# Performance work log

Hardware: AMD Instinct MI355X
Metric: run time of the kernel (lower is better)

The kernel has to match this reference:

```python
import jax, jax.numpy as jnp
import numpy as np

EPS = 1e-5

def _bn_relu(x, g, b, m, v):
    # inference batchnorm + relu, NCHW, fused affine
    scale = g * jax.lax.rsqrt(v + EPS)
    shift = b - m * scale
    return jnp.maximum(x * scale[None, :, None, None] + shift[None, :, None, None], 0.0)

def _conv1x1(x, w):
    # x: [B,C,H,W], w: [O,C]
    return jnp.einsum('bchw,oc->bohw', x, w)

def _xcorr_depthwise(search, kernel, padding=0):
    # search: [B,C,Hs,Ws], kernel: [B,C,Hk,Wk]; grouped conv, groups=B*C
    B, C, Hs, Ws = search.shape
    Hk, Wk = kernel.shape[2], kernel.shape[3]
    x = search.reshape(1, B * C, Hs, Ws)
    k = kernel.reshape(B * C, 1, Hk, Wk)
    out = jax.lax.conv_general_dilated(
        x, k, window_strides=(1, 1), padding=[(padding, padding), (padding, padding)],
        feature_group_count=B * C, dimension_numbers=('NCHW', 'OIHW', 'NCHW'))
    return out.reshape(B, C, out.shape[2], out.shape[3])

def setup_inputs():
    key = jax.random.key(0)
    ks = jax.random.split(key, 20)
    B, Cin, HID, COUT = 128, 256, 256, 20
    s = 1.0 / np.sqrt(Cin)
    inp = {
        'kernel': jax.random.normal(ks[0], (B, Cin, 7, 7), jnp.float32),
        'search': jax.random.normal(ks[1], (B, Cin, 31, 31), jnp.float32),
        # conv_kernel branch (1x1 conv weight stored as [O,C]) + BN stats
        'w_k': jax.random.normal(ks[2], (HID, Cin), jnp.float32) * s,
        'g_k': 1.0 + 0.1 * jax.random.normal(ks[3], (HID,), jnp.float32),
        'b_k': 0.1 * jax.random.normal(ks[4], (HID,), jnp.float32),
        'm_k': 0.1 * jax.random.normal(ks[5], (HID,), jnp.float32),
        'v_k': jax.random.uniform(ks[6], (HID,), jnp.float32, 0.5, 1.5),
        # conv_search branch
        'w_s': jax.random.normal(ks[7], (HID, Cin), jnp.float32) * s,
        'g_s': 1.0 + 0.1 * jax.random.normal(ks[8], (HID,), jnp.float32),
        'b_s': 0.1 * jax.random.normal(ks[9], (HID,), jnp.float32),
        'm_s': 0.1 * jax.random.normal(ks[10], (HID,), jnp.float32),
        'v_s': jax.random.uniform(ks[11], (HID,), jnp.float32, 0.5, 1.5),
        # head: conv1(1x1)+BN+ReLU, conv2(1x1, bias)
        'w_h1': jax.random.normal(ks[12], (HID, HID), jnp.float32) * (1.0 / np.sqrt(HID)),
        'g_h': 1.0 + 0.1 * jax.random.normal(ks[13], (HID,), jnp.float32),
        'b_h': 0.1 * jax.random.normal(ks[14], (HID,), jnp.float32),
        'm_h': 0.1 * jax.random.normal(ks[15], (HID,), jnp.float32),
        'v_h': jax.random.uniform(ks[16], (HID,), jnp.float32, 0.5, 1.5),
        'w_h2': jax.random.normal(ks[17], (COUT, HID), jnp.float32) * (1.0 / np.sqrt(HID)),
        'bias_h2': 0.1 * jax.random.normal(ks[18], (COUT,), jnp.float32),
    }
    return inp

def reference(kernel, search, w_k, g_k, b_k, m_k, v_k, w_s, g_s, b_s, m_s, v_s,
              w_h1, g_h, b_h, m_h, v_h, w_h2, bias_h2):
    k = _bn_relu(_conv1x1(kernel, w_k), g_k, b_k, m_k, v_k)   # [B,256,7,7]
    s = _bn_relu(_conv1x1(search, w_s), g_s, b_s, m_s, v_s)   # [B,256,31,31]
    feat = _xcorr_depthwise(s, k, padding=0)                  # [B,256,25,25]
    y = _bn_relu(_conv1x1(feat, w_h1), g_h, b_h, m_h, v_h)
    out = _conv1x1(y, w_h2) + bias_h2[None, :, None, None]    # [B,20,25,25]
    return out
```

## Files before the change

### kernel.cpp

```cpp
#include <hip/hip_runtime.h>
#include <hip/hip_fp16.h>

typedef _Float16 f16;
typedef __attribute__((ext_vector_type(8))) _Float16 f16x8;
typedef __attribute__((ext_vector_type(4))) _Float16 f16x4;
typedef __attribute__((ext_vector_type(2))) _Float16 f16x2;
typedef __attribute__((ext_vector_type(4))) float f32x4;

#define MFMA16(a, b, c) __builtin_amdgcn_mfma_f32_16x16x32_f16((a), (b), (c), 0, 0, 0)

#define OFF_WK   0u
#define OFF_WS   131072u
#define OFF_WH1  262144u
#define OFF_W2P  393216u
#define OFF_SH   409600u
#define OFF_S    412672u
#define OFF_KF   63392768u

__global__ __launch_bounds__(256) void prep_weights(
    const float* __restrict__ wk, const float* __restrict__ gk, const float* __restrict__ bk,
    const float* __restrict__ mk, const float* __restrict__ vk,
    const float* __restrict__ wsr, const float* __restrict__ gs, const float* __restrict__ bs,
    const float* __restrict__ ms, const float* __restrict__ vs,
    const float* __restrict__ wh1, const float* __restrict__ gh, const float* __restrict__ bh,
    const float* __restrict__ mh, const float* __restrict__ vh,
    const float* __restrict__ wh2,
    f16* __restrict__ wk16, f16* __restrict__ ws16, f16* __restrict__ wh116,
    f16* __restrict__ w2p, float* __restrict__ shifts) {
  int o = blockIdx.x;
  int t = threadIdx.x;
  float sck = gk[o] * rsqrtf(vk[o] + 1e-5f);
  float scs = gs[o] * rsqrtf(vs[o] + 1e-5f);
  float sch = gh[o] * rsqrtf(vh[o] + 1e-5f);
  int idx = o * 256 + t;
  wk16[idx]  = (f16)(wk[idx] * sck);
  ws16[idx]  = (f16)(wsr[idx] * scs);
  wh116[idx] = (f16)(wh1[idx] * sch);
  if (o < 32) w2p[idx] = (o < 20) ? (f16)wh2[idx] : (f16)0;
  if (t == 0) {
    shifts[o]       = bk[o] - mk[o] * sck;
    shifts[256 + o] = bs[o] - ms[o] * scs;
    shifts[512 + o] = bh[o] - mh[o] * sch;
  }
}

__device__ __forceinline__ int pi_row(int q, int r) {
  return (q ^ (r << 2)) + (r << 4);
}
__device__ __forceinline__ int row128(int n) {
  return (n & 64) + pi_row((n >> 2) & 15, n & 3);
}

__global__ __launch_bounds__(512) void conv_nchw128(
    const float* __restrict__ X, const f16* __restrict__ W,
    const float* __restrict__ shift, f16* __restrict__ out) {
  const int C = 256, P = 961;
  int b = blockIdx.x >> 3;
  int ti = blockIdx.x & 7;
  int n0 = ti * 128; if (n0 > P - 128) n0 = P - 128;
  int t = threadIdx.x;
  int w = t >> 6, lane = t & 63;
  int fm = lane & 15, kg = lane >> 4;
  int wo = (w & 3) * 64;
  int wpx = (w >> 2) * 64;

  __shared__ f16 Bs[2][128 * 40];

  int px = (t & 31) * 4;
  int cpr = (t >> 5) * 2;
  const float* xb = X + ((size_t)b * C) * P + n0 + px;

  int wrow[4];
#pragma unroll
  for (int e = 0; e < 4; ++e) wrow[e] = row128(px + e);
  int rrow[4];
#pragma unroll
  for (int nf = 0; nf < 4; ++nf) rrow[nf] = row128(wpx + nf * 16 + fm);

  const f16* wp = W + (size_t)(wo + fm) * C + kg * 8;

  f32x4 rb[3][2];
#pragma unroll
  for (int s = 0; s < 3; ++s) {
    int cl = s * 32 + cpr;
    rb[s][0] = *(const f32x4*)(xb + (size_t)cl * P);
    rb[s][1] = *(const f32x4*)(xb + (size_t)(cl + 1) * P);
  }

  f32x4 acc[4][4] = {};
#pragma unroll
  for (int ci = 0; ci < 8; ++ci) {
    f16x8 a[4];
#pragma unroll
    for (int of = 0; of < 4; ++of)
      a[of] = *(const f16x8*)(wp + (size_t)of * 16 * C + ci * 32);

    f16* buf = Bs[ci & 1];
#pragma unroll
    for (int e = 0; e < 4; ++e) {
      f16x2 v;
      v[0] = (f16)rb[ci % 3][0][e];
      v[1] = (f16)rb[ci % 3][1][e];
      *(f16x2*)&buf[wrow[e] * 40 + cpr] = v;
    }
    if (ci + 3 < 8) {
      int cl = (ci + 3) * 32 + cpr;
      rb[ci % 3][0] = *(const f32x4*)(xb + (size_t)cl * P);
      rb[ci % 3][1] = *(const f32x4*)(xb + (size_t)(cl + 1) * P);
    }
    asm volatile("s_waitcnt lgkmcnt(0)" ::: "memory");
    __builtin_amdgcn_s_barrier();

    f16x8 bfr[4];
#pragma unroll
    for (int nf = 0; nf < 4; ++nf)
      bfr[nf] = *(const f16x8*)&buf[rrow[nf] * 40 + kg * 8];
#pragma unroll
    for (int of = 0; of < 4; ++of)
#pragma unroll
      for (int nf = 0; nf < 4; ++nf)
        acc[of][nf] = MFMA16(a[of], bfr[nf], acc[of][nf]);
  }

#pragma unroll
  for (int of = 0; of < 4; ++of) {
    int orow = wo + of * 16 + kg * 4;
    f32x4 sh = *(const f32x4*)(shift + orow);
#pragma unroll
    for (int nf = 0; nf < 4; ++nf) {
      int n = n0 + wpx + nf * 16 + fm;
      f16x4 st;
#pragma unroll
      for (int r = 0; r < 4; ++r)
        st[r] = (f16)fmaxf(acc[of][nf][r] + sh[r], 0.0f);
      *(f16x4*)(out + ((size_t)b * P + n) * C + orow) = st;
    }
  }
}

template <int P>
__global__ __launch_bounds__(256) void conv_nchw(
    const float* __restrict__ X, const f16* __restrict__ W,
    const float* __restrict__ shift, f16* __restrict__ out) {
  const int C = 256;
  int n0 = blockIdx.x * 64;
  int t = threadIdx.x;
  int lane = t & 63, wave = t >> 6;
  int fm = lane & 15, kg = lane >> 4;

  __shared__ f16 Bs[2][64 * 40];

  int b0 = n0 / P, bp0 = n0 - b0 * P;
  bool safe = (bp0 + 64 <= P);

  int px = (t & 15) * 4;
  int cpr = (t >> 4) * 2;
  const float* xb = X + ((size_t)b0 * C) * P + bp0 + px;

  int ub[4], up[4];
  if (!safe) {
#pragma unroll
    for (int e = 0; e < 4; ++e) {
      int gn = n0 + px + e;
      ub[e] = gn / P;
      up[e] = gn - ub[e] * P;
    }
  }

  int wrow[4];
#pragma unroll
  for (int e = 0; e < 4; ++e) wrow[e] = pi_row(t & 15, e);
  int rrow[4];
#pragma unroll
  for (int nf = 0; nf < 4; ++nf) rrow[nf] = pi_row(nf * 4 + (fm >> 2), fm & 3);

  const f16* wp = W + (size_t)(wave * 64 + fm) * C + kg * 8;

  f32x4 rb[3][2];
#pragma unroll
  for (int s = 0; s < 3; ++s) {
    int cl = s * 32 + cpr;
    if (safe) {
      rb[s][0] = *(const f32x4*)(xb + (size_t)cl * P);
      rb[s][1] = *(const f32x4*)(xb + (size_t)(cl + 1) * P);
    } else {
#pragma unroll
      for (int e = 0; e < 4; ++e) {
        rb[s][0][e] = X[((size_t)ub[e] * C + cl) * P + up[e]];
        rb[s][1][e] = X[((size_t)ub[e] * C + cl + 1) * P + up[e]];
      }
    }
  }

  f32x4 acc[4][4] = {};
#pragma unroll
  for (int ci = 0; ci < 8; ++ci) {
    f16x8 a[4];
#pragma unroll
    for (int of = 0; of < 4; ++of)
      a[of] = *(const f16x8*)(wp + (size_t)of * 16 * C + ci * 32);

    f16* buf = Bs[ci & 1];
#pragma unroll
    for (int e = 0; e < 4; ++e) {
      f16x2 v;
      v[0] = (f16)rb[ci % 3][0][e];
      v[1] = (f16)rb[ci % 3][1][e];
      *(f16x2*)&buf[wrow[e] * 40 + cpr] = v;
    }
    if (ci + 3 < 8) {
      int cl = (ci + 3) * 32 + cpr;
      if (safe) {
        rb[ci % 3][0] = *(const f32x4*)(xb + (size_t)cl * P);
        rb[ci % 3][1] = *(const f32x4*)(xb + (size_t)(cl + 1) * P);
      } else {
#pragma unroll
        for (int e = 0; e < 4; ++e) {
          rb[ci % 3][0][e] = X[((size_t)ub[e] * C + cl) * P + up[e]];
          rb[ci % 3][1][e] = X[((size_t)ub[e] * C + cl + 1) * P + up[e]];
        }
      }
    }
    asm volatile("s_waitcnt lgkmcnt(0)" ::: "memory");
    __builtin_amdgcn_s_barrier();

    f16x8 b[4];
#pragma unroll
    for (int nf = 0; nf < 4; ++nf)
      b[nf] = *(const f16x8*)&buf[rrow[nf] * 40 + kg * 8];
#pragma unroll
    for (int of = 0; of < 4; ++of)
#pragma unroll
      for (int nf = 0; nf < 4; ++nf)
        acc[of][nf] = MFMA16(a[of], b[nf], acc[of][nf]);
  }

#pragma unroll
  for (int of = 0; of < 4; ++of) {
    int orow = wave * 64 + of * 16 + kg * 4;
    f32x4 sh = *(const f32x4*)(shift + orow);
#pragma unroll
    for (int nf = 0; nf < 4; ++nf) {
      int n = n0 + nf * 16 + fm;
      f16x4 st;
#pragma unroll
      for (int r = 0; r < 4; ++r)
        st[r] = (f16)fmaxf(acc[of][nf][r] + sh[r], 0.0f);
      *(f16x4*)(out + (size_t)n * C + orow) = st;
    }
  }
}

__global__ __launch_bounds__(256) void xcorr_head(
    const f16* __restrict__ S ,
    const f16* __restrict__ Kf ,
    const f16* __restrict__ W1, const float* __restrict__ shift,
    const f16* __restrict__ W2p, const float* __restrict__ bias,
    float* __restrict__ out ) {
  const int C = 256;
  int id = blockIdx.x;
  int x = id & 7;
  int r = id >> 3;
  int g = r % 7;
  int b = (r / 7) * 8 + x;

  int t = threadIdx.x;
  int w = t >> 6, lane = t & 63;
  int fm = lane & 15, kg = lane >> 4;
  int oi = g * 4 + w;

  __shared__ char F[100 * 512];

  if (oi < 25) {
    const f16* Sb = S + (size_t)b * 961 * 256 + lane * 4;
    const f16* Kb = Kf + (size_t)b * 49 * 256 + lane * 4;
    f16x4 acc[25] = {};
    for (int di = 0; di < 7; ++di) {
      const f16* sp = Sb + (size_t)(oi + di) * 31 * 256;
      f16x4 srow[31];
#pragma unroll
      for (int j = 0; j < 31; ++j) srow[j] = *(const f16x4*)(sp + (size_t)j * 256);
      const f16* kp = Kb + (size_t)di * 7 * 256;
      f16x4 krow[7];
#pragma unroll
      for (int j = 0; j < 7; ++j) krow[j] = *(const f16x4*)(kp + (size_t)j * 256);
#pragma unroll
      for (int dj = 0; dj < 7; ++dj) {
        f16x4 kv = krow[dj];
#pragma unroll
        for (int oj = 0; oj < 25; ++oj)
          acc[oj] += srow[oj + dj] * kv;
      }
    }
#pragma unroll
    for (int oj = 0; oj < 25; ++oj) {
      int n = w * 25 + oj;
      *(f16x4*)(F + ((n * 512 + lane * 8) ^ ((n & 7) << 4))) = acc[oj];
    }
  } else {
    f16x4 z = {};
#pragma unroll
    for (int oj = 0; oj < 25; ++oj) {
      int n = w * 25 + oj;
      *(f16x4*)(F + ((n * 512 + lane * 8) ^ ((n & 7) << 4))) = z;
    }
  }
  __syncthreads();

  const f16* wp = W1 + (size_t)(w * 64 + fm) * C + kg * 8;
  f32x4 acc1[4][7] = {};
  f16x8 a_cur[4], a_nxt[4];
#pragma unroll
  for (int of = 0; of < 4; ++of)
    a_cur[of] = *(const f16x8*)(wp + (size_t)of * 16 * C);
#pragma unroll
  for (int ci = 0; ci < 8; ++ci) {
    if (ci < 7) {
#pragma unroll
      for (int of = 0; of < 4; ++of)
        a_nxt[of] = *(const f16x8*)(wp + (size_t)of * 16 * C + (ci + 1) * 32);
    }
    f16x8 bf[7];
#pragma unroll
    for (int nf = 0; nf < 7; ++nf) {
      int n = nf * 16 + fm;
      int rn = n < 100 ? n : n - 100;
      bf[nf] = *(const f16x8*)(F + ((rn * 512 + (ci * 32 + kg * 8) * 2) ^ ((rn & 7) << 4)));
    }
    __builtin_amdgcn_s_setprio(1);
#pragma unroll
    for (int of = 0; of < 4; ++of)
#pragma unroll
      for (int nf = 0; nf < 7; ++nf)
        acc1[of][nf] = MFMA16(a_cur[of], bf[nf], acc1[of][nf]);
    __builtin_amdgcn_s_setprio(0);
#pragma unroll
    for (int of = 0; of < 4; ++of) a_cur[of] = a_nxt[of];
  }
  __syncthreads();

#pragma unroll
  for (int of = 0; of < 4; ++of) {
    int orow = w * 64 + of * 16 + kg * 4;
    f32x4 sh = *(const f32x4*)(shift + orow);
#pragma unroll
    for (int nf = 0; nf < 7; ++nf) {
      int n = nf * 16 + fm;
      if (n < 100) {
        f16x4 st;
#pragma unroll
        for (int q = 0; q < 4; ++q)
          st[q] = (f16)fmaxf(acc1[of][nf][q] + sh[q], 0.0f);
        *(f16x4*)(F + ((n * 512 + orow * 2) ^ ((n & 7) << 4))) = st;
      }
    }
  }
  __syncthreads();

  f32x4 acc2[2][2] = {};
  int nfa = w, nfb = w + 4;
  f16x8 w2_cur[2], w2_nxt[2];
  w2_cur[0] = *(const f16x8*)(W2p + (size_t)fm * C + kg * 8);
  w2_cur[1] = *(const f16x8*)(W2p + (size_t)(16 + fm) * C + kg * 8);
#pragma unroll
  for (int ci = 0; ci < 8; ++ci) {
    if (ci < 7) {
      w2_nxt[0] = *(const f16x8*)(W2p + (size_t)fm * C + (ci + 1) * 32 + kg * 8);
      w2_nxt[1] = *(const f16x8*)(W2p + (size_t)(16 + fm) * C + (ci + 1) * 32 + kg * 8);
    }
    int na = nfa * 16 + fm;
    f16x8 b0 = *(const f16x8*)(F + ((na * 512 + (ci * 32 + kg * 8) * 2) ^ ((na & 7) << 4)));
    __builtin_amdgcn_s_setprio(1);
    acc2[0][0] = MFMA16(w2_cur[0], b0, acc2[0][0]);
    acc2[1][0] = MFMA16(w2_cur[1], b0, acc2[1][0]);
    __builtin_amdgcn_s_setprio(0);
    if (nfb < 7) {
      int nb = nfb * 16 + fm;
      int rnb = nb < 100 ? nb : nb - 100;
      f16x8 b1 = *(const f16x8*)(F + ((rnb * 512 + (ci * 32 + kg * 8) * 2) ^ ((rnb & 7) << 4)));
      __builtin_amdgcn_s_setprio(1);
      acc2[0][1] = MFMA16(w2_cur[0], b1, acc2[0][1]);
      acc2[1][1] = MFMA16(w2_cur[1], b1, acc2[1][1]);
      __builtin_amdgcn_s_setprio(0);
    }
    w2_cur[0] = w2_nxt[0];
    w2_cur[1] = w2_nxt[1];
  }

#pragma unroll
  for (int q = 0; q < 2; ++q) {
    int nf = q ? nfb : nfa;
    if (nf >= 7) continue;
    int n = nf * 16 + fm;
    if (n < 100) {
      int oi2 = g * 4 + n / 25;
      int oj2 = n % 25;
      if (oi2 < 25) {
        float* op = out + (size_t)b * 12500 + oi2 * 25 + oj2;
#pragma unroll
        for (int of = 0; of < 2; ++of)
#pragma unroll
          for (int e = 0; e < 4; ++e) {
            int o = of * 16 + kg * 4 + e;
            if (o < 20) op[(size_t)o * 625] = acc2[of][q][e] + bias[o];
          }
      }
    }
  }
}

extern "C" void kernel_launch(void* const* d_in, const int* in_sizes, int n_in,
                              void* d_out, int out_size, void* d_ws, size_t ws_size,
                              hipStream_t stream) {
  const float* kernel_in = (const float*)d_in[0];
  const float* search    = (const float*)d_in[1];
  const float* w_k = (const float*)d_in[2];
  const float* g_k = (const float*)d_in[3];
  const float* b_k = (const float*)d_in[4];
  const float* m_k = (const float*)d_in[5];
  const float* v_k = (const float*)d_in[6];
  const float* w_s = (const float*)d_in[7];
  const float* g_s = (const float*)d_in[8];
  const float* b_s = (const float*)d_in[9];
  const float* m_s = (const float*)d_in[10];
  const float* v_s = (const float*)d_in[11];
  const float* w_h1 = (const float*)d_in[12];
  const float* g_h = (const float*)d_in[13];
  const float* b_h = (const float*)d_in[14];
  const float* m_h = (const float*)d_in[15];
  const float* v_h = (const float*)d_in[16];
  const float* w_h2 = (const float*)d_in[17];
  const float* bias_h2 = (const float*)d_in[18];
  float* out = (float*)d_out;

  char* ws = (char*)d_ws;
  f16* wk16  = (f16*)(ws + OFF_WK);
  f16* ws16  = (f16*)(ws + OFF_WS);
  f16* wh116 = (f16*)(ws + OFF_WH1);
  f16* w2p   = (f16*)(ws + OFF_W2P);
  float* shifts = (float*)(ws + OFF_SH);
  f16* sbuf = (f16*)(ws + OFF_S);
  f16* kbuf = (f16*)(ws + OFF_KF);

  prep_weights<<<256, 256, 0, stream>>>(w_k, g_k, b_k, m_k, v_k,
                                        w_s, g_s, b_s, m_s, v_s,
                                        w_h1, g_h, b_h, m_h, v_h, w_h2,
                                        wk16, ws16, wh116, w2p, shifts);

  conv_nchw128<<<dim3(1024), 512, 0, stream>>>(search, ws16, shifts + 256, sbuf);
  conv_nchw<49><<<dim3(98), 256, 0, stream>>>(kernel_in, wk16, shifts + 0, kbuf);

  xcorr_head<<<dim3(896), 256, 0, stream>>>(
      sbuf, kbuf, wh116, shifts + 512, w2p, bias_h2, out);
}
```

Before: 162.8 us.

## Replace block-tiled search conv with per-wave 16-pixel tiles without barriers

The search-branch 1x1 conv now gives each wave its own independent 16-pixel by 256-output tile, staged through a private LDS slice, so the block-wide barrier and shared 128-pixel tile go away. Each wave loads every weight fragment (16 A fragments per K step) itself and issues scalar strided fp32 loads for its pixels. This removes cross-wave synchronisation and tail waste at the tile level. In exchange it multiplies weight traffic per pixel, makes global loads uncoalesced 4-byte accesses, and raises register pressure with 16 accumulators.

```diff
diff --git a/kernel.cpp b/kernel.cpp
--- a/kernel.cpp
+++ b/kernel.cpp
@@ -47,94 +47,68 @@
 __device__ __forceinline__ int pi_row(int q, int r) {
   return (q ^ (r << 2)) + (r << 4);
 }
-__device__ __forceinline__ int row128(int n) {
-  return (n & 64) + pi_row((n >> 2) & 15, n & 3);
-}
-
-__global__ __launch_bounds__(512) void conv_nchw128(
+
+__global__ __launch_bounds__(512) void conv_wave(
     const float* __restrict__ X, const f16* __restrict__ W,
     const float* __restrict__ shift, f16* __restrict__ out) {
   const int C = 256, P = 961;
-  int b = blockIdx.x >> 3;
-  int ti = blockIdx.x & 7;
-  int n0 = ti * 128; if (n0 > P - 128) n0 = P - 128;
-  int t = threadIdx.x;
-  int w = t >> 6, lane = t & 63;
+  int w = threadIdx.x >> 6;
+  int unit = blockIdx.x * 8 + w;
+  int b = unit / 61;
+  int ti = unit - b * 61;
+  int px0 = ti * 16; if (px0 > P - 16) px0 = P - 16;
+  int lane = threadIdx.x & 63;
   int fm = lane & 15, kg = lane >> 4;
-  int wo = (w & 3) * 64;
-  int wpx = (w >> 2) * 64;
-
-  __shared__ f16 Bs[2][128 * 40];
-
-  int px = (t & 31) * 4;
-  int cpr = (t >> 5) * 2;
-  const float* xb = X + ((size_t)b * C) * P + n0 + px;
-
-  int wrow[4];
-#pragma unroll
-  for (int e = 0; e < 4; ++e) wrow[e] = row128(px + e);
-  int rrow[4];
-#pragma unroll
-  for (int nf = 0; nf < 4; ++nf) rrow[nf] = row128(wpx + nf * 16 + fm);
-
-  const f16* wp = W + (size_t)(wo + fm) * C + kg * 8;
-
-  f32x4 rb[3][2];
-#pragma unroll
-  for (int s = 0; s < 3; ++s) {
-    int cl = s * 32 + cpr;
-    rb[s][0] = *(const f32x4*)(xb + (size_t)cl * P);
-    rb[s][1] = *(const f32x4*)(xb + (size_t)(cl + 1) * P);
-  }
-
-  f32x4 acc[4][4] = {};
+
+  __shared__ f16 SB[8][16 * 40];
+  f16* mylds = SB[w];
+
+  const float* xb = X + ((size_t)b * C + (size_t)kg * 8) * P + px0 + fm;
+
+  float rb[3][8];
+#pragma unroll
+  for (int s = 0; s < 3; ++s)
+#pragma unroll
+    for (int j = 0; j < 8; ++j)
+      rb[s][j] = xb[((size_t)s * 32 + j) * P];
+
+  f32x4 acc[16] = {};
 #pragma unroll
   for (int ci = 0; ci < 8; ++ci) {
-    f16x8 a[4];
-#pragma unroll
-    for (int of = 0; of < 4; ++of)
-      a[of] = *(const f16x8*)(wp + (size_t)of * 16 * C + ci * 32);
-
-    f16* buf = Bs[ci & 1];
-#pragma unroll
-    for (int e = 0; e < 4; ++e) {
-      f16x2 v;
-      v[0] = (f16)rb[ci % 3][0][e];
-      v[1] = (f16)rb[ci % 3][1][e];
-      *(f16x2*)&buf[wrow[e] * 40 + cpr] = v;
-    }
+    f16x8 v;
+#pragma unroll
+    for (int j = 0; j < 8; ++j) v[j] = (f16)rb[ci % 3][j];
+    *(f16x8*)&mylds[fm * 40 + kg * 8] = v;
+
     if (ci + 3 < 8) {
-      int cl = (ci + 3) * 32 + cpr;
-      rb[ci % 3][0] = *(const f32x4*)(xb + (size_t)cl * P);
-      rb[ci % 3][1] = *(const f32x4*)(xb + (size_t)(cl + 1) * P);
-    }
+#pragma unroll
+      for (int j = 0; j < 8; ++j)
+        rb[ci % 3][j] = xb[((size_t)(ci + 3) * 32 + j) * P];
+    }
+
+    f16x8 a[16];
+#pragma unroll
+    for (int of = 0; of < 16; ++of)
+      a[of] = *(const f16x8*)(W + (size_t)(of * 16 + fm) * C + ci * 32 + kg * 8);
+
     asm volatile("s_waitcnt lgkmcnt(0)" ::: "memory");
-    __builtin_amdgcn_s_barrier();
-
-    f16x8 bfr[4];
-#pragma unroll
-    for (int nf = 0; nf < 4; ++nf)
-      bfr[nf] = *(const f16x8*)&buf[rrow[nf] * 40 + kg * 8];
-#pragma unroll
-    for (int of = 0; of < 4; ++of)
-#pragma unroll
-      for (int nf = 0; nf < 4; ++nf)
-        acc[of][nf] = MFMA16(a[of], bfr[nf], acc[of][nf]);
-  }
-
-#pragma unroll
-  for (int of = 0; of < 4; ++of) {
-    int orow = wo + of * 16 + kg * 4;
+    f16x8 bf = *(const f16x8*)&mylds[fm * 40 + kg * 8 +
+                                     0];
+#pragma unroll
+    for (int of = 0; of < 16; ++of)
+      acc[of] = MFMA16(a[of], bf, acc[of]);
+  }
+
+  size_t nrow = (size_t)b * P + px0 + fm;
+#pragma unroll
+  for (int of = 0; of < 16; ++of) {
+    int orow = of * 16 + kg * 4;
     f32x4 sh = *(const f32x4*)(shift + orow);
-#pragma unroll
-    for (int nf = 0; nf < 4; ++nf) {
-      int n = n0 + wpx + nf * 16 + fm;
-      f16x4 st;
-#pragma unroll
-      for (int r = 0; r < 4; ++r)
-        st[r] = (f16)fmaxf(acc[of][nf][r] + sh[r], 0.0f);
-      *(f16x4*)(out + ((size_t)b * P + n) * C + orow) = st;
-    }
+    f16x4 st;
+#pragma unroll
+    for (int r = 0; r < 4; ++r)
+      st[r] = (f16)fmaxf(acc[of][r] + sh[r], 0.0f);
+    *(f16x4*)(out + nrow * C + orow) = st;
   }
 }
 
@@ -447,7 +421,7 @@
                                         w_h1, g_h, b_h, m_h, v_h, w_h2,
                                         wk16, ws16, wh116, w2p, shifts);
 
-  conv_nchw128<<<dim3(1024), 512, 0, stream>>>(search, ws16, shifts + 256, sbuf);
+  conv_wave<<<dim3(976), 512, 0, stream>>>(search, ws16, shifts + 256, sbuf);
   conv_nchw<49><<<dim3(98), 256, 0, stream>>>(kernel_in, wk16, shifts + 0, kbuf);
 
   xcorr_head<<<dim3(896), 256, 0, stream>>>(
```

Result: slower. 241.5 us (+48.4%).

## Stream search tile into LDS with direct global-to-LDS loads in search conv

Applied to the files above, without the earlier changes.

Replaces register-staged loading of the search input (fp32 load, fp16 convert, swizzled LDS store) with buffer loads that write fp32 directly into a double-buffered LDS tile. The fp16 conversion moves to the LDS read side, where each lane gathers 8 scalar floats per fragment. This is meant to cut VGPR pressure and instruction count on the load path and to overlap the next tile's fetch with MFMA work. In exchange it doubles the LDS footprint, and the strided scalar LDS reads may cause bank conflicts and extra conversion work.

```diff
diff --git a/kernel.cpp b/kernel.cpp
--- a/kernel.cpp
+++ b/kernel.cpp
@@ -8,6 +8,11 @@
 typedef __attribute__((ext_vector_type(4))) float f32x4;
 
 #define MFMA16(a, b, c) __builtin_amdgcn_mfma_f32_16x16x32_f16((a), (b), (c), 0, 0, 0)
+
+#define GL16(SRC, DST)                                                        \
+  __builtin_amdgcn_global_load_lds(                                           \
+      (const __attribute__((address_space(1))) unsigned int*)(SRC),           \
+      (__attribute__((address_space(3))) unsigned int*)(DST), 16, 0, 0)
 
 #define OFF_WK   0u
 #define OFF_WS   131072u
@@ -47,11 +52,8 @@
 __device__ __forceinline__ int pi_row(int q, int r) {
   return (q ^ (r << 2)) + (r << 4);
 }
-__device__ __forceinline__ int row128(int n) {
-  return (n & 64) + pi_row((n >> 2) & 15, n & 3);
-}
-
-__global__ __launch_bounds__(512) void conv_nchw128(
+
+__global__ __launch_bounds__(512) void conv_gl(
     const float* __restrict__ X, const f16* __restrict__ W,
     const float* __restrict__ shift, f16* __restrict__ out) {
   const int C = 256, P = 961;
@@ -64,62 +66,47 @@
   int wo = (w & 3) * 64;
   int wpx = (w >> 2) * 64;
 
-  __shared__ f16 Bs[2][128 * 40];
-
-  int px = (t & 31) * 4;
-  int cpr = (t >> 5) * 2;
-  const float* xb = X + ((size_t)b * C) * P + n0 + px;
-
-  int wrow[4];
-#pragma unroll
-  for (int e = 0; e < 4; ++e) wrow[e] = row128(px + e);
-  int rrow[4];
-#pragma unroll
-  for (int nf = 0; nf < 4; ++nf) rrow[nf] = row128(wpx + nf * 16 + fm);
+  __shared__ float Bs[2][32 * 128];
+
+  const float* s_src0 = X + ((size_t)b * C + 4 * w + (lane >> 5)) * P + n0 + (lane & 31) * 4;
 
   const f16* wp = W + (size_t)(wo + fm) * C + kg * 8;
 
-  f32x4 rb[3][2];
-#pragma unroll
-  for (int s = 0; s < 3; ++s) {
-    int cl = s * 32 + cpr;
-    rb[s][0] = *(const f32x4*)(xb + (size_t)cl * P);
-    rb[s][1] = *(const f32x4*)(xb + (size_t)(cl + 1) * P);
-  }
+  GL16(s_src0,         &Bs[0][(4 * w) * 128]);
+  GL16(s_src0 + 2 * P, &Bs[0][(4 * w + 2) * 128]);
 
   f32x4 acc[4][4] = {};
 #pragma unroll
   for (int ci = 0; ci < 8; ++ci) {
+    float* buf = Bs[ci & 1];
+    if (ci < 7) {
+      const float* s = s_src0 + (size_t)(ci + 1) * 32 * P;
+      float* d = Bs[(ci + 1) & 1];
+      GL16(s,         &d[(4 * w) * 128]);
+      GL16(s + 2 * P, &d[(4 * w + 2) * 128]);
+      asm volatile("s_waitcnt vmcnt(2)" ::: "memory");
+    } else {
+      asm volatile("s_waitcnt vmcnt(0)" ::: "memory");
+    }
+    __builtin_amdgcn_s_barrier();
+
     f16x8 a[4];
 #pragma unroll
     for (int of = 0; of < 4; ++of)
       a[of] = *(const f16x8*)(wp + (size_t)of * 16 * C + ci * 32);
 
-    f16* buf = Bs[ci & 1];
-#pragma unroll
-    for (int e = 0; e < 4; ++e) {
-      f16x2 v;
-      v[0] = (f16)rb[ci % 3][0][e];
-      v[1] = (f16)rb[ci % 3][1][e];
-      *(f16x2*)&buf[wrow[e] * 40 + cpr] = v;
-    }
-    if (ci + 3 < 8) {
-      int cl = (ci + 3) * 32 + cpr;
-      rb[ci % 3][0] = *(const f32x4*)(xb + (size_t)cl * P);
-      rb[ci % 3][1] = *(const f32x4*)(xb + (size_t)(cl + 1) * P);
-    }
-    asm volatile("s_waitcnt lgkmcnt(0)" ::: "memory");
+#pragma unroll
+    for (int nf = 0; nf < 4; ++nf) {
+      int pxc = wpx + nf * 16 + fm;
+      f16x8 bf;
+#pragma unroll
+      for (int j = 0; j < 8; ++j)
+        bf[j] = (f16)buf[(kg * 8 + j) * 128 + pxc];
+#pragma unroll
+      for (int of = 0; of < 4; ++of)
+        acc[of][nf] = MFMA16(a[of], bf, acc[of][nf]);
+    }
     __builtin_amdgcn_s_barrier();
-
-    f16x8 bfr[4];
-#pragma unroll
-    for (int nf = 0; nf < 4; ++nf)
-      bfr[nf] = *(const f16x8*)&buf[rrow[nf] * 40 + kg * 8];
-#pragma unroll
-    for (int of = 0; of < 4; ++of)
-#pragma unroll
-      for (int nf = 0; nf < 4; ++nf)
-        acc[of][nf] = MFMA16(a[of], bfr[nf], acc[of][nf]);
   }
 
 #pragma unroll
@@ -447,7 +434,7 @@
                                         w_h1, g_h, b_h, m_h, v_h, w_h2,
                                         wk16, ws16, wh116, w2p, shifts);
 
-  conv_nchw128<<<dim3(1024), 512, 0, stream>>>(search, ws16, shifts + 256, sbuf);
+  conv_gl<<<dim3(1024), 512, 0, stream>>>(search, ws16, shifts + 256, sbuf);
   conv_nchw<49><<<dim3(98), 256, 0, stream>>>(kernel_in, wk16, shifts + 0, kbuf);
 
   xcorr_head<<<dim3(896), 256, 0, stream>>>(
```

After: 160.4 us, median of 2. Within noise of the previous version (-1.5%).
